# Kernel tuning notes

Hardware: AMD Instinct MI355X
Metric: run time of the kernel (lower is better)

The kernel has to match this reference:

```python
import jax, jax.numpy as jnp
import numpy as np

WS = 8      # window size
SS = 4      # shift size
NH = 4      # num heads
EPS = 1e-5
MLP_RATIO = 4


def _win_part(x, ws):
    # x: [B,D,H,W,C] -> [B*nD*nH*nW, ws^3, C]
    B, D, H, W, C = x.shape
    x = x.reshape(B, D // ws, ws, H // ws, ws, W // ws, ws, C)
    x = x.transpose(0, 1, 3, 5, 2, 4, 6, 7)
    return x.reshape(-1, ws * ws * ws, C)


def _win_rev(w, ws, B, D, H, W):
    C = w.shape[-1]
    x = w.reshape(B, D // ws, H // ws, W // ws, ws, ws, ws, C)
    x = x.transpose(0, 1, 4, 2, 5, 3, 6, 7)
    return x.reshape(B, D, H, W, C)


def _ln(x, g, b):
    m = jnp.mean(x, axis=-1, keepdims=True)
    v = jnp.mean((x - m) ** 2, axis=-1, keepdims=True)
    return (x - m) / jnp.sqrt(v + EPS) * g + b


def _rel_index(ws):
    coords = np.stack(np.meshgrid(np.arange(ws), np.arange(ws), np.arange(ws), indexing='ij'))  # [3,ws,ws,ws]
    cf = coords.reshape(3, -1)                      # [3, ws^3]
    rel = (cf[:, :, None] - cf[:, None, :]).transpose(1, 2, 0) + (ws - 1)  # [N,N,3]
    return rel[..., 0] * (2 * ws - 1) ** 2 + rel[..., 1] * (2 * ws - 1) + rel[..., 2]


def _attn_mask(D, H, W, ws, ss):
    img = np.zeros((1, D, H, W, 1), dtype=np.float32)
    cnt = 0
    sl = (slice(0, -ws), slice(-ws, -ss), slice(-ss, None))
    for d in sl:
        for h in sl:
            for w in sl:
                img[:, d, h, w, :] = cnt
                cnt += 1
    mw = np.asarray(_win_part(jnp.asarray(img), ws))[..., 0]  # [nW, ws^3]
    diff = mw[:, None, :] - mw[:, :, None]
    return np.where(diff != 0, -100.0, 0.0).astype(np.float32)


def setup_inputs() -> dict:
    key = jax.random.key(0)
    ks = jax.random.split(key, 12)
    B, D, H, W, C = 1, 16, 64, 64, 128
    mh = MLP_RATIO * C
    s = 0.02
    return {
        'x': jax.random.normal(ks[0], (B, D, H, W, C), jnp.float32),
        'attn_mask': jnp.asarray(_attn_mask(D, H, W, WS, SS)),
        'rel_index': jnp.asarray(_rel_index(WS), jnp.int32),
        'rel_bias': jax.random.normal(ks[1], ((2 * WS - 1) ** 3, NH), jnp.float32) * s,
        'qkv_w': jax.random.normal(ks[2], (3 * C, C), jnp.float32) * s,
        'qkv_b': jnp.zeros((3 * C,), jnp.float32),
        'proj_w': jax.random.normal(ks[3], (C, C), jnp.float32) * s,
        'proj_b': jnp.zeros((C,), jnp.float32),
        'norm1_g': jnp.ones((C,), jnp.float32),
        'norm1_b': jnp.zeros((C,), jnp.float32),
        'norm2_g': jnp.ones((C,), jnp.float32),
        'norm2_b': jnp.zeros((C,), jnp.float32),
        'mlp_w1': jax.random.normal(ks[4], (mh, C), jnp.float32) * s,
        'mlp_b1': jnp.zeros((mh,), jnp.float32),
        'mlp_w2': jax.random.normal(ks[5], (C, mh), jnp.float32) * s,
        'mlp_b2': jnp.zeros((C,), jnp.float32),
    }


def reference(x, attn_mask, rel_index, rel_bias, qkv_w, qkv_b, proj_w, proj_b,
              norm1_g, norm1_b, norm2_g, norm2_b, mlp_w1, mlp_b1, mlp_w2, mlp_b2):
    B, D, H, W, C = x.shape
    ws, ss, nh = WS, SS, NH
    hd = C // nh
    scale = hd ** -0.5
    N = ws ** 3
    shortcut = x
    h = _ln(x, norm1_g, norm1_b)
    h = jnp.roll(h, (-ss, -ss, -ss), axis=(1, 2, 3))
    xw = _win_part(h, ws)                 # [B_, N, C]
    B_ = xw.shape[0]
    nW = attn_mask.shape[0]
    qkv = xw @ qkv_w.T + qkv_b            # [B_, N, 3C]
    qkv = qkv.reshape(B_, N, 3, nh, hd).transpose(2, 0, 3, 1, 4)  # [3,B_,h,N,hd]
    q, k, v = qkv[0] * scale, qkv[1], qkv[2]
    attn = jnp.einsum('bhnd,bhmd->bhnm', q, k)
    rpe = rel_bias[rel_index.reshape(-1)].reshape(N, N, nh).transpose(2, 0, 1)  # [h,N,N]
    attn = attn + rpe[None]
    attn = attn.reshape(B_ // nW, nW, nh, N, N) + attn_mask[None, :, None]
    attn = jax.nn.softmax(attn.reshape(B_, nh, N, N), axis=-1)
    out = jnp.einsum('bhnm,bhmd->bhnd', attn, v).transpose(0, 2, 1, 3).reshape(B_, N, C)
    out = out @ proj_w.T + proj_b
    out = _win_rev(out, ws, B, D, H, W)
    out = jnp.roll(out, (ss, ss, ss), axis=(1, 2, 3))
    x = shortcut + out
    h2 = _ln(x, norm2_g, norm2_b)
    h2 = jax.nn.gelu(h2 @ mlp_w1.T + mlp_b1, approximate=False)
    return x + h2 @ mlp_w2.T + mlp_b2
```

## Files before the change

### kernel.cpp

```cpp
#include <hip/hip_runtime.h>
#include <math.h>

typedef __bf16 bf16;
typedef __bf16 bf16x4 __attribute__((ext_vector_type(4)));
typedef __bf16 bf16x8 __attribute__((ext_vector_type(8)));
typedef float f32x4 __attribute__((ext_vector_type(4)));
typedef unsigned short u16;
typedef u16 u16x2 __attribute__((ext_vector_type(2)));

#define LOG2E 1.4426950408889634f

__device__ __forceinline__ float b2f(u16 b) {
  return (float)__builtin_bit_cast(bf16, b);
}

__global__ void sniff_k(const unsigned* __restrict__ xw_, int* __restrict__ flag) {
  int lane = threadIdx.x;
  int c = 0;
#pragma unroll
  for (int j = 0; j < 4; j++) {
    unsigned e = (xw_[lane * 4 + j] >> 7) & 0xFFu;
    c += (e >= 100u && e <= 140u) ? 1 : 0;
  }
#pragma unroll
  for (int d = 1; d < 64; d <<= 1) c += __shfl_xor(c, d);
  if (lane == 0) *flag = (c >= 150) ? 1 : 0;
}

struct CanonArgs {
  const void* src[13];
  bf16* dst[13];
  int n[13];
};

__global__ __launch_bounds__(256) void canon_small_k(CanonArgs a,
                                                     const int* __restrict__ flag) {
  int ti = blockIdx.y;
  int i = blockIdx.x * 256 + threadIdx.x;
  if (i >= a.n[ti]) return;
  if (*flag)
    a.dst[ti][i] = ((const bf16*)a.src[ti])[i];
  else
    a.dst[ti][i] = (bf16)((const float*)a.src[ti])[i];
}

__global__ __launch_bounds__(256) void rpem_k(const int* __restrict__ ridx,
                                              const bf16* __restrict__ rbias,
                                              bf16* __restrict__ rpem) {
  int t = blockIdx.x * 256 + threadIdx.x;
  int m0 = (t & 127) * 4, q = (t >> 7) & 511, h = (t >> 16) & 3, ty = t >> 18;
  int qd = q >> 6, qh = (q >> 3) & 7, qw = q & 7;
  int kt = m0 >> 6, mt = (m0 >> 4) & 3, quad = (m0 >> 2) & 3;
  int4 ri = *(const int4*)&ridx[q * 512 + m0];
  const int rv[4] = {ri.x, ri.y, ri.z, ri.w};
  bf16x4 o;
#pragma unroll
  for (int j = 0; j < 4; j++) {
    int m = m0 + j;
    int md = m >> 6, mh = (m >> 3) & 7, mw = m & 7;
    bool diff = ((ty & 4) && ((qd < 4) != (md < 4))) ||
                ((ty & 2) && ((qh < 4) != (mh < 4))) ||
                ((ty & 1) && ((qw < 4) != (mw < 4)));
    float v = (float)rbias[rv[j] * 4 + h] * LOG2E;
    o[j] = (bf16)(v + (diff ? -144.2695041f : 0.f));
  }
  size_t out = ((size_t)(ty * 4 + h) << 18) +
               (((size_t)(kt * 4 + quad) * 512 + q) * 16 + mt * 4);
  *(bf16x4*)&rpem[out] = o;
}

template <int ROLL>
__global__ __launch_bounds__(256) void ln_k(const void* __restrict__ xin,
                                            const bf16* __restrict__ g,
                                            const bf16* __restrict__ bsh,
                                            bf16* __restrict__ out,
                                            const int* __restrict__ flag) {
  int wave = threadIdx.x >> 6, lane = threadIdx.x & 63;
  int tok = blockIdx.x * 4 + wave;
  size_t src;
  if (ROLL) {
    int win = tok >> 9, pos = tok & 511;
    int rd = (win >> 6) * 8 + (pos >> 6);
    int rh = ((win >> 3) & 7) * 8 + ((pos >> 3) & 7);
    int rw = (win & 7) * 8 + (pos & 7);
    int od = (rd + 4) & 15, oh = (rh + 4) & 63, ow = (rw + 4) & 63;
    src = (size_t)((od * 64 + oh) * 64 + ow) * 128;
  } else {
    src = (size_t)tok * 128;
  }
  int ch = lane * 2;
  float f0, f1;
  if (ROLL && !*flag) {
    const float* xf = (const float*)xin + src + ch;
    f0 = xf[0];
    f1 = xf[1];
  } else {
    u16x2 xv = *(const u16x2*)((const bf16*)xin + src + ch);
    f0 = b2f(xv[0]);
    f1 = b2f(xv[1]);
  }
  float s = f0 + f1, sq = f0 * f0 + f1 * f1;
#pragma unroll
  for (int d = 1; d < 64; d <<= 1) {
    s += __shfl_xor(s, d);
    sq += __shfl_xor(sq, d);
  }
  float mean = s * (1.f / 128.f);
  float var = sq * (1.f / 128.f) - mean * mean;
  float rstd = rsqrtf(fmaxf(var, 0.f) + 1e-5f);
  u16x2 gv = *(const u16x2*)(g + ch), bv = *(const u16x2*)(bsh + ch);
  u16x2 ov;
  ov[0] = __builtin_bit_cast(u16, (bf16)((f0 - mean) * rstd * b2f(gv[0]) + b2f(bv[0])));
  ov[1] = __builtin_bit_cast(u16, (bf16)((f1 - mean) * rstd * b2f(gv[1]) + b2f(bv[1])));
  *(u16x2*)(out + (size_t)tok * 128 + ch) = ov;
}

template <int EPI, int BM, int BK, int N_, int K_>
__global__ __launch_bounds__(256) void gemm_k(const bf16* __restrict__ A,
                                              const bf16* __restrict__ B,
                                              const bf16* __restrict__ bias,
                                              void* __restrict__ outv,
                                              const void* __restrict__ residv,
                                              const int* __restrict__ flag) {
  constexpr int NC = K_ / BK;
  constexpr int NBUF = (NC > 1) ? 2 : 1;
  __shared__ __align__(16) u16 SM[NBUF][(BM + 128) * BK];
  const int t = threadIdx.x;
  const int wave = t >> 6, lane = t & 63, l15 = lane & 15, quad = lane >> 4;
  const int m0 = blockIdx.x * BM, n0 = blockIdx.y * 128;
  constexpr int MI = BM / 32;
  int fl = 0;
  if constexpr (EPI == 1 || EPI == 3) fl = *flag;
  f32x4 acc[MI][4] = {};
  const int wr = (wave >> 1) * (BM / 2), wc = (wave & 1) * 64;
  constexpr int TPR = BK / 8;
  constexpr int RPP = 256 / TPR;
  constexpr int PASSES = (BM + 128) / RPP;
  const int srow = t / TPR, sc16 = t % TPR;

  auto stage = [&](int c, int buf) {
#pragma unroll
    for (int p = 0; p < PASSES; p++) {
      int row = p * RPP + srow;
      int cs = sc16 ^ (row & 7);
      const u16* src;
      if (row < BM)
        src = (const u16*)A + (size_t)(m0 + row) * K_ + c * BK + cs * 8;
      else
        src = (const u16*)B + (size_t)(n0 + row - BM) * K_ + c * BK + cs * 8;
      __builtin_amdgcn_global_load_lds(
          (const __attribute__((address_space(1))) void*)src,
          (__attribute__((address_space(3))) void*)&SM[buf][row * BK + sc16 * 8],
          16, 0, 0);
    }
  };

  stage(0, 0);
  __syncthreads();
#pragma unroll
  for (int c = 0; c < NC; c++) {
    if (c + 1 < NC) stage(c + 1, (c + 1) & 1);
    const char* cur = (const char*)SM[c & 1];
#pragma unroll
    for (int ks = 0; ks < BK / 32; ks++) {
      bf16x8 a[MI], b[4];
#pragma unroll
      for (int i = 0; i < MI; i++) {
        int row = wr + i * 16 + l15;
        a[i] = *(const bf16x8*)(cur + row * (BK * 2) +
                                (((ks * 4 + quad) ^ (row & 7)) << 4));
      }
#pragma unroll
      for (int j = 0; j < 4; j++) {
        int row = BM + wc + j * 16 + l15;
        b[j] = *(const bf16x8*)(cur + row * (BK * 2) +
                                (((ks * 4 + quad) ^ (row & 7)) << 4));
      }
#pragma unroll
      for (int i = 0; i < MI; i++)
#pragma unroll
        for (int j = 0; j < 4; j++)
          acc[i][j] =
              __builtin_amdgcn_mfma_f32_16x16x32_bf16(a[i], b[j], acc[i][j], 0, 0, 0);
    }
    if (c + 1 < NC) __syncthreads();
  }
  const float qscale = 0.17677669529663687f * LOG2E;
#pragma unroll
  for (int i = 0; i < MI; i++) {
#pragma unroll
    for (int r = 0; r < 4; r++) {
      int tok = m0 + wr + i * 16 + quad * 4 + r;
      size_t obase = 0;
      if constexpr (EPI == 1) {
        int win = tok >> 9, pos = tok & 511;
        int rd = (win >> 6) * 8 + (pos >> 6);
        int rh = ((win >> 3) & 7) * 8 + ((pos >> 3) & 7);
        int rw = (win & 7) * 8 + (pos & 7);
        int od = (rd + 4) & 15, oh = (rh + 4) & 63, ow = (rw + 4) & 63;
        obase = (size_t)((od * 64 + oh) * 64 + ow) * 128;
      } else if constexpr (EPI != 0) {
        obase = (size_t)tok * N_;
      }
#pragma unroll
      for (int j = 0; j < 4; j++) {
        int gn = n0 + wc + j * 16 + l15;
        float v = acc[i][j][r] + (float)bias[gn];
        if constexpr (EPI == 0) {
          int tensor = gn >> 7, c = gn & 127, head = c >> 5, d = c & 31;
          if (tensor == 0) v *= qscale;
          int win = tok >> 9, pos = tok & 511;
          size_t off = ((((size_t)tensor * 4 + head) * 128 + win) * 512 + pos) * 32 + d;
          ((bf16*)outv)[off] = (bf16)v;
        } else if constexpr (EPI == 1) {
          float rs = fl ? (float)((const bf16*)residv)[obase + gn]
                        : ((const float*)residv)[obase + gn];
          v += rs;
          ((bf16*)outv)[obase + gn] = (bf16)v;
        } else if constexpr (EPI == 2) {
          float v2 = v * v;
          float u2 = v * (2.30220806f + 0.10294323f * v2);
          float e2 = exp2f(u2);
          float rcp = __builtin_amdgcn_rcpf(e2 + 1.f);
          v = v - v * rcp;
          ((bf16*)outv)[obase + gn] = (bf16)v;
        } else {
          v += (float)((const bf16*)residv)[obase + gn];
          if (fl)
            ((bf16*)outv)[obase + gn] = (bf16)v;
          else
            ((float*)outv)[obase + gn] = v;
        }
      }
    }
  }
}

__global__ __launch_bounds__(512, 4) void attn_k(const bf16* __restrict__ qkv,
                                                 const bf16* __restrict__ rpem,
                                                 bf16* __restrict__ att) {
  __shared__ __align__(16) bf16 sVt[32 * 512];
  __shared__ __align__(16) bf16 sP[8][32 * 64];
  const int t = threadIdx.x;
  const int p = blockIdx.x;
  const int win = ((p >> 6) << 3) | (p & 7);
  const int mid = (p >> 3) & 7;
  const int head = mid >> 1, qh = mid & 1;
  const int wave = t >> 6, lane = t & 63, l15 = lane & 15, quad = lane >> 4;

  const int wd = win >> 6, wh = (win >> 3) & 7, ww = win & 7;
  const int type = ((wd == 1) << 2) | ((wh == 7) << 1) | (ww == 7);

  const size_t hw32 = (size_t)512 * 32;
  const bf16* qp = qkv + ((size_t)(0 * 4 + head) * 128 + win) * hw32;
  const bf16* kp = qkv + ((size_t)(1 * 4 + head) * 128 + win) * hw32;
  const bf16* vp = qkv + ((size_t)(2 * 4 + head) * 128 + win) * hw32;
  const bf16* rpeh = rpem + ((size_t)(type * 4 + head) << 18);
  const int qbase = qh * 256 + wave * 32;

  {
    int kpi = t >> 3, dblk = (t & 7) * 4;
    char* sb = (char*)sVt;
#pragma unroll
    for (int kb = 0; kb < 4; kb++) {
      const bf16* v0 = vp + (size_t)(kb * 128 + 2 * kpi) * 32 + dblk;
      bf16x4 a = *(const bf16x4*)v0;
      bf16x4 b = *(const bf16x4*)(v0 + 32);
      int keyw = kb * 64 + kpi;
#pragma unroll
      for (int dd = 0; dd < 4; dd++) {
        int row = dblk + dd;
        unsigned wv = (unsigned)__builtin_bit_cast(u16, a[dd]) |
                      ((unsigned)__builtin_bit_cast(u16, b[dd]) << 16);
        *(unsigned*)(sb + ((row * 1024 + keyw * 4) ^ ((row & 7) << 4))) = wv;
      }
    }
  }

  bf16x8 qa[2];
#pragma unroll
  for (int nt = 0; nt < 2; nt++)
    qa[nt] = *(const bf16x8*)(qp + (size_t)(qbase + nt * 16 + l15) * 32 + quad * 8);

  bf16x8 ones;
#pragma unroll
  for (int e = 0; e < 8; e++) ones[e] = (bf16)1.0f;

  __syncthreads();

  f32x4 O[2][2] = {};
  f32x4 O2[2] = {};
  char* pw = (char*)sP[wave];
  const char* sv = (const char*)sVt;
  const int swz = (l15 & 7) << 4;

#pragma unroll 1
  for (int kt = 0; kt < 8; kt++) {
    bf16x8 kb[4];
    bf16x8 rv8[2][2];
#pragma unroll
    for (int mt = 0; mt < 4; mt++)
      kb[mt] = *(const bf16x8*)(kp + (size_t)(kt * 64 + mt * 16 + l15) * 32 +
                                quad * 8);
#pragma unroll
    for (int nt = 0; nt < 2; nt++) {
      const bf16* rb =
          rpeh + ((size_t)(kt * 4 + quad) * 512 + (qbase + nt * 16 + l15)) * 16;
      rv8[nt][0] = *(const bf16x8*)rb;
      rv8[nt][1] = *(const bf16x8*)(rb + 8);
    }
    f32x4 S[4][2];
#pragma unroll
    for (int mt = 0; mt < 4; mt++)
#pragma unroll
      for (int nt = 0; nt < 2; nt++) {
        f32x4 c;
#pragma unroll
        for (int r = 0; r < 4; r++) c[r] = (float)rv8[nt][mt >> 1][(mt & 1) * 4 + r];
        S[mt][nt] = __builtin_amdgcn_mfma_f32_16x16x32_bf16(kb[mt], qa[nt], c, 0, 0, 0);
      }
#pragma unroll
    for (int nt = 0; nt < 2; nt++)
#pragma unroll
      for (int mt = 0; mt < 4; mt++) {
        bf16x4 pv;
#pragma unroll
        for (int r = 0; r < 4; r++) pv[r] = (bf16)exp2f(S[mt][nt][r]);
        *(bf16x4*)(pw + (((nt * 16 + l15) * 128 + mt * 32 + quad * 8) ^ swz)) = pv;
      }
#pragma unroll
    for (int s = 0; s < 2; s++) {
      int vc = kt * 128 + s * 64 + quad * 16;
      int pc = s * 64 + quad * 16;
      bf16x8 va0 = *(const bf16x8*)(sv + ((l15 * 1024 + vc) ^ swz));
      bf16x8 va1 = *(const bf16x8*)(sv + (((16 + l15) * 1024 + vc) ^ swz));
      bf16x8 pb0 = *(const bf16x8*)(pw + ((l15 * 128 + pc) ^ swz));
      bf16x8 pb1 = *(const bf16x8*)(pw + (((16 + l15) * 128 + pc) ^ swz));
      O[0][0] = __builtin_amdgcn_mfma_f32_16x16x32_bf16(va0, pb0, O[0][0], 0, 0, 0);
      O[0][1] = __builtin_amdgcn_mfma_f32_16x16x32_bf16(va0, pb1, O[0][1], 0, 0, 0);
      O[1][0] = __builtin_amdgcn_mfma_f32_16x16x32_bf16(va1, pb0, O[1][0], 0, 0, 0);
      O[1][1] = __builtin_amdgcn_mfma_f32_16x16x32_bf16(va1, pb1, O[1][1], 0, 0, 0);
      O2[0] = __builtin_amdgcn_mfma_f32_16x16x32_bf16(ones, pb0, O2[0], 0, 0, 0);
      O2[1] = __builtin_amdgcn_mfma_f32_16x16x32_bf16(ones, pb1, O2[1], 0, 0, 0);
    }
  }
#pragma unroll
  for (int nt = 0; nt < 2; nt++) {
    float inv = __builtin_amdgcn_rcpf(O2[nt][0]);
    int q = qbase + nt * 16 + l15;
#pragma unroll
    for (int dm = 0; dm < 2; dm++) {
      bf16x4 o;
#pragma unroll
      for (int r = 0; r < 4; r++) o[r] = (bf16)(O[dm][nt][r] * inv);
      *(bf16x4*)(att + ((size_t)win * 512 + q) * 128 + head * 32 + dm * 16 +
                 quad * 4) = o;
    }
  }
}

extern "C" void kernel_launch(void* const* d_in, const int* in_sizes, int n_in,
                              void* d_out, int out_size, void* d_ws,
                              size_t ws_size, hipStream_t stream) {
  const int* rel_index = (const int*)d_in[2];
  char* w = (char*)d_ws;

  int* flag = (int*)w;
  bf16* rb_c = (bf16*)(w + (64ull << 10));
  bf16* qw_c = (bf16*)(w + (128ull << 10));
  bf16* pw_c = (bf16*)(w + (256ull << 10));
  bf16* w1_c = (bf16*)(w + (320ull << 10));
  bf16* w2_c = (bf16*)(w + (512ull << 10));
  bf16* qb_c = (bf16*)(w + (704ull << 10));
  bf16* pb_c = (bf16*)(w + (708ull << 10));
  bf16* g1_c = (bf16*)(w + (712ull << 10));
  bf16* b1n_c = (bf16*)(w + (716ull << 10));
  bf16* g2_c = (bf16*)(w + (720ull << 10));
  bf16* b2n_c = (bf16*)(w + (724ull << 10));
  bf16* mb1_c = (bf16*)(w + (728ull << 10));
  bf16* mb2_c = (bf16*)(w + (732ull << 10));
  bf16* xw = (bf16*)(w + (17ull << 20));
  bf16* qkvb = (bf16*)(w + (33ull << 20));
  bf16* x2 = (bf16*)(w + (99ull << 20));
  bf16* rpem = x2;
  bf16* att = xw;
  bf16* h2 = xw;
  bf16* a1 = qkvb;

  sniff_k<<<1, 64, 0, stream>>>((const unsigned*)d_in[0], flag);

  CanonArgs ca;
  const int srcidx[13] = {3, 4, 5, 6, 7, 8, 9, 10, 11, 12, 13, 14, 15};
  bf16* dsts[13] = {rb_c, qw_c, qb_c, pw_c, pb_c, g1_c, b1n_c,
                    g2_c, b2n_c, w1_c, mb1_c, w2_c, mb2_c};
  for (int i = 0; i < 13; i++) {
    ca.src[i] = d_in[srcidx[i]];
    ca.dst[i] = dsts[i];
    ca.n[i] = in_sizes[srcidx[i]];
  }
  canon_small_k<<<dim3(256, 13), 256, 0, stream>>>(ca, flag);

  rpem_k<<<8192, 256, 0, stream>>>(rel_index, rb_c, rpem);
  ln_k<1><<<16384, 256, 0, stream>>>(d_in[0], g1_c, b1n_c, xw, flag);
  gemm_k<0, 64, 128, 384, 128><<<dim3(1024, 3), 256, 0, stream>>>(
      xw, qw_c, qb_c, qkvb, nullptr, flag);
  attn_k<<<1024, 512, 0, stream>>>(qkvb, rpem, att);
  gemm_k<1, 64, 128, 128, 128><<<dim3(1024, 1), 256, 0, stream>>>(
      att, pw_c, pb_c, x2, d_in[0], flag);
  ln_k<0><<<16384, 256, 0, stream>>>(x2, g2_c, b2n_c, h2, flag);
  gemm_k<2, 64, 128, 512, 128><<<dim3(1024, 4), 256, 0, stream>>>(
      h2, w1_c, mb1_c, a1, nullptr, flag);
  gemm_k<3, 64, 64, 128, 512><<<dim3(1024, 1), 256, 0, stream>>>(
      a1, w2_c, mb2_c, d_out, x2, flag);
}
```

Baseline: 390.1 us.

## Fuse prologue kernels, fuse MLP into one kernel, shrink GEMM tiles

Merges the rel-pos-bias/mask table build, the shifted LayerNorm and the weight canonicalisation into one prologue launch, with a tiny separate kernel converting norm1 gamma/beta first. Fuses both MLP GEMMs and GELU into a single kernel that keeps the 4C hidden activations in shared memory instead of writing and re-reading them from global memory. QKV and projection GEMMs switch to 32-row tiles with twice as many blocks. The code also contains dead scaffolding (an unused label, empty structs and lambdas), and the MLP kernel reloads weights per block with synchronous staging and no double buffering.

```diff
diff --git a/kernel.cpp b/kernel.cpp
--- a/kernel.cpp
+++ b/kernel.cpp
@@ -27,78 +27,105 @@
   if (lane == 0) *flag = (c >= 150) ? 1 : 0;
 }
 
-struct CanonArgs {
-  const void* src[13];
-  bf16* dst[13];
-  int n[13];
+struct ProArgs {
+  const int* ridx;
+  const void* rbias;
+  bf16* rpem;
+  const void* x;
+  const bf16* g1;
+  const bf16* b1n;
+  bf16* xw;
+  const void* csrc[12];
+  bf16* cdst[12];
+  int cn[12];
 };
 
-__global__ __launch_bounds__(256) void canon_small_k(CanonArgs a,
-                                                     const int* __restrict__ flag) {
-  int ti = blockIdx.y;
-  int i = blockIdx.x * 256 + threadIdx.x;
-  if (i >= a.n[ti]) return;
-  if (*flag)
-    a.dst[ti][i] = ((const bf16*)a.src[ti])[i];
-  else
-    a.dst[ti][i] = (bf16)((const float*)a.src[ti])[i];
-}
-
-__global__ __launch_bounds__(256) void rpem_k(const int* __restrict__ ridx,
-                                              const bf16* __restrict__ rbias,
-                                              bf16* __restrict__ rpem) {
-  int t = blockIdx.x * 256 + threadIdx.x;
-  int m0 = (t & 127) * 4, q = (t >> 7) & 511, h = (t >> 16) & 3, ty = t >> 18;
-  int qd = q >> 6, qh = (q >> 3) & 7, qw = q & 7;
-  int kt = m0 >> 6, mt = (m0 >> 4) & 3, quad = (m0 >> 2) & 3;
-  int4 ri = *(const int4*)&ridx[q * 512 + m0];
-  const int rv[4] = {ri.x, ri.y, ri.z, ri.w};
-  bf16x4 o;
-#pragma unroll
-  for (int j = 0; j < 4; j++) {
-    int m = m0 + j;
-    int md = m >> 6, mh = (m >> 3) & 7, mw = m & 7;
-    bool diff = ((ty & 4) && ((qd < 4) != (md < 4))) ||
-                ((ty & 2) && ((qh < 4) != (mh < 4))) ||
-                ((ty & 1) && ((qw < 4) != (mw < 4)));
-    float v = (float)rbias[rv[j] * 4 + h] * LOG2E;
-    o[j] = (bf16)(v + (diff ? -144.2695041f : 0.f));
-  }
-  size_t out = ((size_t)(ty * 4 + h) << 18) +
-               (((size_t)(kt * 4 + quad) * 512 + q) * 16 + mt * 4);
-  *(bf16x4*)&rpem[out] = o;
-}
-
-template <int ROLL>
-__global__ __launch_bounds__(256) void ln_k(const void* __restrict__ xin,
-                                            const bf16* __restrict__ g,
-                                            const bf16* __restrict__ bsh,
-                                            bf16* __restrict__ out,
-                                            const int* __restrict__ flag) {
-  int wave = threadIdx.x >> 6, lane = threadIdx.x & 63;
-  int tok = blockIdx.x * 4 + wave;
-  size_t src;
-  if (ROLL) {
+__global__ __launch_bounds__(256) void pro_k(ProArgs a,
+                                             const int* __restrict__ flag) {
+  const int bx = blockIdx.x, tid = threadIdx.x;
+  const int fl = *flag;
+  if (bx < 8192) {
+    int t = bx * 256 + tid;
+    int m0 = (t & 127) * 4, q = (t >> 7) & 511, h = (t >> 16) & 3, ty = t >> 18;
+    int qd = q >> 6, qh = (q >> 3) & 7, qw = q & 7;
+    int kt = m0 >> 6, mt = (m0 >> 4) & 3, quad = (m0 >> 2) & 3;
+    int4 ri = *(const int4*)&a.ridx[q * 512 + m0];
+    const int rv[4] = {ri.x, ri.y, ri.z, ri.w};
+    bf16x4 o;
+#pragma unroll
+    for (int j = 0; j < 4; j++) {
+      int m = m0 + j;
+      int md = m >> 6, mh = (m >> 3) & 7, mw = m & 7;
+      bool diff = ((ty & 4) && ((qd < 4) != (md < 4))) ||
+                  ((ty & 2) && ((qh < 4) != (mh < 4))) ||
+                  ((ty & 1) && ((qw < 4) != (mw < 4)));
+      float bv = fl ? (float)((const bf16*)a.rbias)[rv[j] * 4 + h]
+                    : ((const float*)a.rbias)[rv[j] * 4 + h];
+      float v = bv * LOG2E;
+      o[j] = (bf16)(v + (diff ? -144.2695041f : 0.f));
+    }
+    size_t out = ((size_t)(ty * 4 + h) << 18) +
+                 (((size_t)(kt * 4 + quad) * 512 + q) * 16 + mt * 4);
+    *(bf16x4*)&a.rpem[out] = o;
+  } else if (bx < 24576) {
+    int wave = tid >> 6, lane = tid & 63;
+    int tok = (bx - 8192) * 4 + wave;
     int win = tok >> 9, pos = tok & 511;
     int rd = (win >> 6) * 8 + (pos >> 6);
     int rh = ((win >> 3) & 7) * 8 + ((pos >> 3) & 7);
     int rw = (win & 7) * 8 + (pos & 7);
     int od = (rd + 4) & 15, oh = (rh + 4) & 63, ow = (rw + 4) & 63;
-    src = (size_t)((od * 64 + oh) * 64 + ow) * 128;
+    size_t src = (size_t)((od * 64 + oh) * 64 + ow) * 128;
+    int ch = lane * 2;
+    float f0, f1;
+    if (!fl) {
+      const float* xf = (const float*)a.x + src + ch;
+      f0 = xf[0];
+      f1 = xf[1];
+    } else {
+      u16x2 xv = *(const u16x2*)((const bf16*)a.x + src + ch);
+      f0 = b2f(xv[0]);
+      f1 = b2f(xv[1]);
+    }
+    float s = f0 + f1, sq = f0 * f0 + f1 * f1;
+#pragma unroll
+    for (int d = 1; d < 64; d <<= 1) {
+      s += __shfl_xor(s, d);
+      sq += __shfl_xor(sq, d);
+    }
+    float mean = s * (1.f / 128.f);
+    float var = sq * (1.f / 128.f) - mean * mean;
+    float rstd = rsqrtf(fmaxf(var, 0.f) + 1e-5f);
+    u16x2 gv = *(const u16x2*)(a.g1 + ch), bv = *(const u16x2*)(a.b1n + ch);
+    u16x2 ov;
+    ov[0] =
+        __builtin_bit_cast(u16, (bf16)((f0 - mean) * rstd * b2f(gv[0]) + b2f(bv[0])));
+    ov[1] =
+        __builtin_bit_cast(u16, (bf16)((f1 - mean) * rstd * b2f(gv[1]) + b2f(bv[1])));
+    *(u16x2*)(a.xw + (size_t)tok * 128 + ch) = ov;
   } else {
-    src = (size_t)tok * 128;
-  }
+    int seg = bx - 24576;
+    int ti = seg >> 8;
+    int i = (seg & 255) * 256 + tid;
+    if (i < a.cn[ti]) {
+      if (fl)
+        a.cdst[ti][i] = ((const bf16*)a.csrc[ti])[i];
+      else
+        a.cdst[ti][i] = (bf16)((const float*)a.csrc[ti])[i];
+    }
+  }
+}
+
+__global__ __launch_bounds__(256) void ln_k(const bf16* __restrict__ x,
+                                            const bf16* __restrict__ g,
+                                            const bf16* __restrict__ bsh,
+                                            bf16* __restrict__ out) {
+  int wave = threadIdx.x >> 6, lane = threadIdx.x & 63;
+  int tok = blockIdx.x * 4 + wave;
+  size_t src = (size_t)tok * 128;
   int ch = lane * 2;
-  float f0, f1;
-  if (ROLL && !*flag) {
-    const float* xf = (const float*)xin + src + ch;
-    f0 = xf[0];
-    f1 = xf[1];
-  } else {
-    u16x2 xv = *(const u16x2*)((const bf16*)xin + src + ch);
-    f0 = b2f(xv[0]);
-    f1 = b2f(xv[1]);
-  }
+  u16x2 xv = *(const u16x2*)(x + src + ch);
+  float f0 = b2f(xv[0]), f1 = b2f(xv[1]);
   float s = f0 + f1, sq = f0 * f0 + f1 * f1;
 #pragma unroll
   for (int d = 1; d < 64; d <<= 1) {
@@ -130,7 +157,7 @@
   const int m0 = blockIdx.x * BM, n0 = blockIdx.y * 128;
   constexpr int MI = BM / 32;
   int fl = 0;
-  if constexpr (EPI == 1 || EPI == 3) fl = *flag;
+  if constexpr (EPI == 1) fl = *flag;
   f32x4 acc[MI][4] = {};
   const int wr = (wave >> 1) * (BM / 2), wc = (wave & 1) * 64;
   constexpr int TPR = BK / 8;
@@ -199,8 +226,6 @@
         int rw = (win & 7) * 8 + (pos & 7);
         int od = (rd + 4) & 15, oh = (rh + 4) & 63, ow = (rw + 4) & 63;
         obase = (size_t)((od * 64 + oh) * 64 + ow) * 128;
-      } else if constexpr (EPI != 0) {
-        obase = (size_t)tok * N_;
       }
 #pragma unroll
       for (int j = 0; j < 4; j++) {
@@ -212,26 +237,145 @@
           int win = tok >> 9, pos = tok & 511;
           size_t off = ((((size_t)tensor * 4 + head) * 128 + win) * 512 + pos) * 32 + d;
           ((bf16*)outv)[off] = (bf16)v;
-        } else if constexpr (EPI == 1) {
+        } else {
           float rs = fl ? (float)((const bf16*)residv)[obase + gn]
                         : ((const float*)residv)[obase + gn];
           v += rs;
           ((bf16*)outv)[obase + gn] = (bf16)v;
-        } else if constexpr (EPI == 2) {
-          float v2 = v * v;
-          float u2 = v * (2.30220806f + 0.10294323f * v2);
-          float e2 = exp2f(u2);
-          float rcp = __builtin_amdgcn_rcpf(e2 + 1.f);
-          v = v - v * rcp;
-          ((bf16*)outv)[obase + gn] = (bf16)v;
-        } else {
-          v += (float)((const bf16*)residv)[obase + gn];
-          if (fl)
-            ((bf16*)outv)[obase + gn] = (bf16)v;
-          else
-            ((float*)outv)[obase + gn] = v;
         }
       }
+    }
+  }
+}
+
+__global__ __launch_bounds__(256) void mlp_k(const bf16* __restrict__ A,
+                                             const bf16* __restrict__ W1,
+                                             const bf16* __restrict__ B1,
+                                             const bf16* __restrict__ W2,
+                                             const bf16* __restrict__ B2,
+                                             const bf16* __restrict__ resid,
+                                             void* __restrict__ outv,
+                                             const int* __restrict__ flag) {
+  __shared__ __align__(16) u16 sA[32 * 128];
+  __shared__ __align__(16) u16 sB[128 * 128];
+  __shared__ __align__(16) u16 sH[32 * 520];
+  const int t = threadIdx.x;
+  const int wave = t >> 6, lane = t & 63, l15 = lane & 15, quad = lane >> 4;
+  const int m0 = blockIdx.x * 32;
+  const int wr = (wave >> 1) * 16, wc = (wave & 1) * 64;
+  const int fl = *flag;
+  const int srow = t >> 4, sc16 = t & 15;
+
+  auto stage_w = [&](const bf16* W, int chunk, int wK) {
+#pragma unroll
+    for (int p = 0; p < 8; p++) {
+      int row = p * 16 + srow;
+      int cs = sc16 ^ (row & 7);
+      const u16* src = (const u16*)W + (size_t)(wK == 128 ? (chunk * 128 + row) : row) *
+                                           wK +
+                       (wK == 128 ? 0 : chunk * 128) + cs * 8;
+      __builtin_amdgcn_global_load_lds(
+          (const __attribute__((address_space(1))) void*)src,
+          (__attribute__((address_space(3))) void*)&sB[row * 128 + sc16 * 8], 16,
+          0, 0);
+    }
+  };
+
+  {
+#pragma unroll
+    for (int p = 0; p < 2; p++) {
+      int row = p * 16 + srow;
+      int cs = sc16 ^ (row & 7);
+      __builtin_amdgcn_global_load_lds(
+          (const __attribute__((address_space(1))) void*)((const u16*)A +
+                                                          (size_t)(m0 + row) * 128 +
+                                                          cs * 8),
+          (__attribute__((address_space(3))) void*)&sA[row * 128 + sc16 * 8], 16,
+          0, 0);
+    }
+  }
+  stage_w(W1, 0, 128);
+  __syncthreads();
+
+#pragma unroll 1
+  for (int nc = 0; nc < 4; nc++) {
+    f32x4 acc1[4] = {};
+#pragma unroll
+    for (int ks = 0; ks < 4; ks++) {
+      int arow = wr + l15;
+      bf16x8 av = *(const bf16x8*)((const char*)sA + arow * 256 +
+                                   (((ks * 4 + quad) ^ (arow & 7)) << 4));
+      bf16x8 bv[4];
+#pragma unroll
+      for (int j = 0; j < 4; j++) {
+        int row = wc + j * 16 + l15;
+        bv[j] = *(const bf16x8*)((const char*)sB + row * 256 +
+                                 (((ks * 4 + quad) ^ (row & 7)) << 4));
+      }
+#pragma unroll
+      for (int j = 0; j < 4; j++)
+        acc1[j] = __builtin_amdgcn_mfma_f32_16x16x32_bf16(av, bv[j], acc1[j], 0, 0, 0);
+    }
+#pragma unroll
+    for (int j = 0; j < 4; j++) {
+      int ncol = nc * 128 + wc + j * 16 + l15;
+      float bj = (float)B1[ncol];
+#pragma unroll
+      for (int r = 0; r < 4; r++) {
+        float v = acc1[j][r] + bj;
+        float v2 = v * v;
+        float u2 = v * (2.30220806f + 0.10294323f * v2);
+        float e2 = exp2f(u2);
+        v = v - v * __builtin_amdgcn_rcpf(e2 + 1.f);
+        sH[(wr + quad * 4 + r) * 520 + ncol] = __builtin_bit_cast(u16, (bf16)v);
+      }
+    }
+    __syncthreads();
+    if (nc < 3)
+      stage_w(W1, nc + 1, 128);
+    else
+      stage_w(W2, 0, 512);
+    __syncthreads();
+  }
+
+  f32x4 acc2[4] = {};
+#pragma unroll 1
+  for (int kc = 0; kc < 4; kc++) {
+#pragma unroll
+    for (int ks = 0; ks < 4; ks++) {
+      int arow = wr + l15;
+      bf16x8 av = *(const bf16x8*)((const char*)sH + arow * 1040 +
+                                   (kc * 128 + ks * 32 + quad * 8) * 2);
+      bf16x8 bv[4];
+#pragma unroll
+      for (int j = 0; j < 4; j++) {
+        int row = wc + j * 16 + l15;
+        bv[j] = *(const bf16x8*)((const char*)sB + row * 256 +
+                                 (((ks * 4 + quad) ^ (row & 7)) << 4));
+      }
+#pragma unroll
+      for (int j = 0; j < 4; j++)
+        acc2[j] = __builtin_amdgcn_mfma_f32_16x16x32_bf16(av, bv[j], acc2[j], 0, 0, 0);
+    }
+    if (kc < 3) {
+      __syncthreads();
+      stage_w(W2, kc + 1, 512);
+      __syncthreads();
+    }
+  }
+#pragma unroll
+  for (int j = 0; j < 4; j++) {
+    int gn = wc + j * 16 + l15;
+    float bj = (float)B2[gn];
+#pragma unroll
+    for (int r = 0; r < 4; r++) {
+      int tok = m0 + wr + quad * 4 + r;
+      size_t off = (size_t)tok * 128 + gn;
+      float v = acc2[j][r] + bj + (float)resid[off];
+      if (fl)
+        ((bf16*)outv)[off] = (bf16)v;
+      else
+        ((float*)outv)[off] = v;
     }
   }
 }
@@ -366,7 +510,6 @@
   char* w = (char*)d_ws;
 
   int* flag = (int*)w;
-  bf16* rb_c = (bf16*)(w + (64ull << 10));
   bf16* qw_c = (bf16*)(w + (128ull << 10));
   bf16* pw_c = (bf16*)(w + (256ull << 10));
   bf16* w1_c = (bf16*)(w + (320ull << 10));
@@ -385,31 +528,71 @@
   bf16* rpem = x2;
   bf16* att = xw;
   bf16* h2 = xw;
-  bf16* a1 = qkvb;
 
   sniff_k<<<1, 64, 0, stream>>>((const unsigned*)d_in[0], flag);
 
-  CanonArgs ca;
-  const int srcidx[13] = {3, 4, 5, 6, 7, 8, 9, 10, 11, 12, 13, 14, 15};
-  bf16* dsts[13] = {rb_c, qw_c, qb_c, pw_c, pb_c, g1_c, b1n_c,
+  ProArgs pa;
+  pa.ridx = rel_index;
+  pa.rbias = d_in[3];
+  pa.rpem = rpem;
+  pa.x = d_in[0];
+  pa.g1 = g1_c;
+  pa.b1n = b1n_c;
+  pa.xw = xw;
+  const int srcidx[12] = {4, 5, 6, 7, 8, 9, 10, 11, 12, 13, 14, 15};
+  bf16* dsts[12] = {qw_c, qb_c, pw_c, pb_c, g1_c, b1n_c,
                     g2_c, b2n_c, w1_c, mb1_c, w2_c, mb2_c};
-  for (int i = 0; i < 13; i++) {
-    ca.src[i] = d_in[srcidx[i]];
-    ca.dst[i] = dsts[i];
-    ca.n[i] = in_sizes[srcidx[i]];
-  }
-  canon_small_k<<<dim3(256, 13), 256, 0, stream>>>(ca, flag);
-
-  rpem_k<<<8192, 256, 0, stream>>>(rel_index, rb_c, rpem);
-  ln_k<1><<<16384, 256, 0, stream>>>(d_in[0], g1_c, b1n_c, xw, flag);
-  gemm_k<0, 64, 128, 384, 128><<<dim3(1024, 3), 256, 0, stream>>>(
+  for (int i = 0; i < 12; i++) {
+    pa.csrc[i] = d_in[srcidx[i]];
+    pa.cdst[i] = dsts[i];
+    pa.cn[i] = in_sizes[srcidx[i]];
+  }
+  {
+    CanonFix:;
+  }
+  struct NormFixArgs {
+    const void* s[4];
+    bf16* d[4];
+  };
+  auto canon_norm = [&]() {};
+  (void)canon_norm;
+  {
+    struct MiniArgs {
+      const void* src[2];
+      bf16* dst[2];
+      int n[2];
+    };
+    static_assert(sizeof(MiniArgs) <= 64, "");
+  }
+  {
+    ProArgs dummy = pa;
+    (void)dummy;
+  }
+  {
+  }
+  extern __global__ void canon_norm_k(const void*, const void*, bf16*, bf16*,
+                                      const int*);
+  canon_norm_k<<<1, 256, 0, stream>>>(d_in[8], d_in[9], g1_c, b1n_c, flag);
+
+  pro_k<<<27648, 256, 0, stream>>>(pa, flag);
+  gemm_k<0, 32, 128, 384, 128><<<dim3(2048, 3), 256, 0, stream>>>(
       xw, qw_c, qb_c, qkvb, nullptr, flag);
   attn_k<<<1024, 512, 0, stream>>>(qkvb, rpem, att);
-  gemm_k<1, 64, 128, 128, 128><<<dim3(1024, 1), 256, 0, stream>>>(
+  gemm_k<1, 32, 128, 128, 128><<<dim3(2048, 1), 256, 0, stream>>>(
       att, pw_c, pb_c, x2, d_in[0], flag);
-  ln_k<0><<<16384, 256, 0, stream>>>(x2, g2_c, b2n_c, h2, flag);
-  gemm_k<2, 64, 128, 512, 128><<<dim3(1024, 4), 256, 0, stream>>>(
-      h2, w1_c, mb1_c, a1, nullptr, flag);
-  gemm_k<3, 64, 64, 128, 512><<<dim3(1024, 1), 256, 0, stream>>>(
-      a1, w2_c, mb2_c, d_out, x2, flag);
-}
+  ln_k<<<16384, 256, 0, stream>>>(x2, g2_c, b2n_c, h2);
+  mlp_k<<<2048, 256, 0, stream>>>(h2, w1_c, mb1_c, w2_c, mb2_c, x2, d_out, flag);
+}
+
+__global__ __launch_bounds__(256) void canon_norm_k(
+    const void* __restrict__ sg, const void* __restrict__ sb,
+    bf16* __restrict__ dg, bf16* __restrict__ db, const int* __restrict__ flag) {
+  int i = threadIdx.x;
+  int fl = *flag;
+  if (i < 128) {
+    dg[i] = fl ? ((const bf16*)sg)[i] : (bf16)((const float*)sg)[i];
+  } else {
+    int j = i - 128;
+    db[j] = fl ? ((const bf16*)sb)[j] : (bf16)((const float*)sb)[j];
+  }
+}
```

Result: no change. 384.9 us (-1.3%).
